# Kernel tuning notes

Measured on AMD Instinct MI355X. Metric: run time of the kernel, lower is better.

## Reference

```python
import jax, jax.numpy as jnp
import numpy as np

ALPHA = 1.0
MIN_FEATURE_SIZE = 1.0
SC = 1e-12                      # stabilizer added to first derivatives
EPS_V_FLOOR = 1e-32 / 6.0       # torch.tensor(1e-32 ** 1 / 6) == 1e-32/6 (** binds tighter than /)


def _grad2d(phi, d):
    """Vectorized equivalent of numerical_gradient_2d: central differences in the
    interior, one-sided forward/backward differences at the boundaries."""
    gx = jnp.concatenate([
        (phi[1:2, :] - phi[0:1, :]) / d,           # forward diff at i == 0
        (phi[2:, :] - phi[:-2, :]) / (2.0 * d),    # central diff in interior
        (phi[-1:, :] - phi[-2:-1, :]) / d,         # backward diff at i == H-1
    ], axis=0)
    gy = jnp.concatenate([
        (phi[:, 1:2] - phi[:, 0:1]) / d,
        (phi[:, 2:] - phi[:, :-2]) / (2.0 * d),
        (phi[:, -1:] - phi[:, -2:-1]) / d,
    ], axis=1)
    return gx, gy


def setup_inputs() -> dict:
    key = jax.random.key(0)
    eps = jax.random.normal(key, (4096, 4096), dtype=jnp.float32)
    grid_size = jnp.asarray(0.05, dtype=jnp.float32)
    return {"eps": eps, "grid_size": grid_size}


def reference(eps, grid_size):
    # mirror the field along axis 1 (torch.cat((eps, eps.flip(1)), dim=1)) -> [H, 2W]
    eps = jnp.concatenate([eps, eps[:, ::-1]], axis=1)

    # ls_derivatives: first derivatives (+SC), then second derivatives of those
    eps_x, eps_y = _grad2d(eps, grid_size)
    eps_x = eps_x + SC
    eps_y = eps_y + SC
    eps_xx, eps_xy = _grad2d(eps_x, grid_size)
    _, eps_yy = _grad2d(eps_y, grid_size)

    pi_d = np.pi / (1.1 * MIN_FEATURE_SIZE)
    eps_v = jnp.maximum(jnp.sqrt(eps_x**2 + eps_y**2), EPS_V_FLOOR)
    k = (eps_x**2 * eps_yy - 2.0 * eps_x * eps_y * eps_xy + eps_y**2 * eps_xx) / eps_v**3
    curve_const = jnp.abs(k * jnp.arctan(eps_v / eps)) - pi_d
    return jnp.nansum(ALPHA * jnp.maximum(curve_const, 0.0) * grid_size**2)
```

## Files before the change

kernel.cpp:

```cpp
#include <hip/hip_runtime.h>
#include <math.h>


#define BLOCK_X 256
#define ROWS_PER 16

__device__ __forceinline__ float fast_atan_ratio(float v, float c, float rv)
{
    const float rc = __builtin_amdgcn_rcpf(c);
    const float q  = v * rc;
    const float iq = c * rv;
    const bool  big = fabsf(q) > 1.0f;
    const float t  = big ? iq : q;
    const float s  = t * t;
    float p = fmaf(s, -0.01172120f, 0.05265332f);
    p = fmaf(s, p, -0.11643287f);
    p = fmaf(s, p,  0.19354346f);
    p = fmaf(s, p, -0.33262347f);
    p = fmaf(s, p,  0.99997726f);
    const float at = p * t;
    const float hp = copysignf(1.57079632679f, q);
    return big ? (hp - at) : at;
}

template<bool INT>
__device__ __forceinline__ float compute_rows(
    const float* __restrict__ eps, int Hn, int Wn, int i0,
    int j, int jm, int jmm, int cjp, int cjpp,
    float rd, float syj, float sym, float syp)
{
    const float rd2 = 0.5f * rd;
    const float SC = 1e-12f;
    const float FLOORV = (float)(1e-32 / 6.0);
    const float pi_d = 3.14159265358979323846f / 1.1f;

    float acc = 0.0f;
    for (int r = 0; r < ROWS_PER; ++r) {
        const int i = i0 + r;
        int im, ip, imm, ipp;
        float sxi, sxm, sxp;
        if (INT) {
            im = i - 1; ip = i + 1; imm = i - 2; ipp = i + 2;
            sxi = rd2; sxm = rd2; sxp = rd2;
        } else {
            im  = (i > 0) ? i - 1 : 0;
            ip  = (i < Hn - 1) ? i + 1 : Hn - 1;
            imm = (im > 0) ? im - 1 : 0;
            ipp = (ip < Hn - 1) ? ip + 1 : Hn - 1;
            sxi = (i == 0 || i == Hn - 1) ? rd : rd2;
            sxm = (im == 0) ? rd : rd2;
            sxp = (ip == Hn - 1) ? rd : rd2;
        }

        const float* rowc  = eps + (size_t)i   * (size_t)Wn;
        const float* rown  = eps + (size_t)im  * (size_t)Wn;
        const float* rows_ = eps + (size_t)ip  * (size_t)Wn;
        const float* rownn = eps + (size_t)imm * (size_t)Wn;
        const float* rowss = eps + (size_t)ipp * (size_t)Wn;

        const float e_c  = rowc[j];
        const float e_n  = rown[j],   e_s  = rows_[j];
        const float e_nn = rownn[j],  e_ss = rowss[j];
        const float e_w  = rowc[jm],  e_e  = rowc[cjp];
        const float e_ww = rowc[jmm], e_ee = rowc[cjpp];
        const float e_nw = rown[jm],  e_ne = rown[cjp];
        const float e_sw = rows_[jm], e_se = rows_[cjp];

        const float ex = fmaf(e_s - e_n, sxi, SC);
        const float ey = fmaf(e_e - e_w, syj, SC);

        float exn = fmaf(e_c - e_nn, sxm, SC);
        float exs = fmaf(e_ss - e_c, sxp, SC);
        if (!INT) {
            if (i == 0)      exn = ex;
            if (i == Hn - 1) exs = ex;
        }
        const float exx = (exs - exn) * sxi;

        float eyw = fmaf(e_c - e_ww, sym, SC);
        const float eye = fmaf(e_ee - e_c, syp, SC);
        if (j == 0) eyw = ey;
        const float eyy = (eye - eyw) * syj;

        const float exy = ((e_se - e_ne) - (e_sw - e_nw)) * (sxi * syj);

        const float t1 = ex * ex;
        const float t2 = ey * ey;
        float num = t1 * eyy;
        num = fmaf(t2, exx, num);
        num = fmaf(-2.0f * (ex * ey), exy, num);

        float ev = __builtin_amdgcn_sqrtf(t1 + t2);
        ev = fmaxf(ev, FLOORV);
        const float rv = __builtin_amdgcn_rcpf(ev);
        const float k  = num * (rv * rv) * rv;
        const float at = fast_atan_ratio(ev, e_c, rv);
        const float cc = fabsf(k * at) - pi_d;
        acc += fmaxf(cc, 0.0f);
    }
    return acc;
}

__global__ __launch_bounds__(BLOCK_X) void curve_partial_kernel(
    const float* __restrict__ eps, const float* __restrict__ gs,
    double* __restrict__ partial, int Hn, int Wn)
{
    const int tx = threadIdx.x;
    const int j  = blockIdx.x * BLOCK_X + tx;
    const int i0 = blockIdx.y * ROWS_PER;
    const float d  = gs[0];
    const float rd = 1.0f / d;
    const float rd2 = 0.5f * rd;

    float accf = 0.0f;
    {
        const int jm  = (j > 0) ? j - 1 : 0;
        const int jmm = (j > 1) ? j - 2 : 0;
        const int jp = j + 1, jpp = j + 2;
        const int cjp  = (jp  < Wn) ? jp  : (2 * Wn - 1 - jp);
        const int cjpp = (jpp < Wn) ? jpp : (2 * Wn - 1 - jpp);
        const float syj = (j == 0)  ? rd : rd2;
        const float sym = (jm == 0) ? rd : rd2;
        const float syp = rd2;

        const bool interior = (i0 >= 2) && (i0 + ROWS_PER + 1 < Hn);
        if (interior)
            accf = compute_rows<true >(eps, Hn, Wn, i0, j, jm, jmm, cjp, cjpp, rd, syj, sym, syp);
        else
            accf = compute_rows<false>(eps, Hn, Wn, i0, j, jm, jmm, cjp, cjpp, rd, syj, sym, syp);
    }

    double acc = (double)accf;
    #pragma unroll
    for (int off = 32; off > 0; off >>= 1)
        acc += __shfl_down(acc, off, 64);
    __shared__ double lds[BLOCK_X / 64];
    const int lane = tx & 63, wv = tx >> 6;
    if (lane == 0) lds[wv] = acc;
    __syncthreads();
    if (tx == 0) {
        partial[blockIdx.y * gridDim.x + blockIdx.x] =
            lds[0] + lds[1] + lds[2] + lds[3];
    }
}

__global__ __launch_bounds__(256) void curve_finish_kernel(
    const double* __restrict__ partial, int n,
    const float* __restrict__ gs, float* __restrict__ out)
{
    const int tx = threadIdx.x;
    double acc = 0.0;
    for (int idx = tx; idx < n; idx += 256) acc += partial[idx];
    #pragma unroll
    for (int off = 32; off > 0; off >>= 1)
        acc += __shfl_down(acc, off, 64);
    __shared__ double lds[4];
    const int lane = tx & 63, wv = tx >> 6;
    if (lane == 0) lds[wv] = acc;
    __syncthreads();
    if (tx == 0) {
        const double d = (double)gs[0];
        out[0] = (float)((lds[0] + lds[1] + lds[2] + lds[3]) * 2.0 * d * d);
    }
}

extern "C" void kernel_launch(void* const* d_in, const int* in_sizes, int n_in,
                              void* d_out, int out_size, void* d_ws, size_t ws_size,
                              hipStream_t stream) {
    const float* eps = (const float*)d_in[0];
    const float* gs  = (const float*)d_in[1];
    float* out = (float*)d_out;

    const int n = in_sizes[0];
    int Wn = (int)(sqrt((double)n) + 0.5);
    int Hn = n / Wn;

    const int gx = (Wn + BLOCK_X - 1) / BLOCK_X;
    const int gy = (Hn + ROWS_PER - 1) / ROWS_PER;
    double* partial = (double*)d_ws;

    curve_partial_kernel<<<dim3(gx, gy), BLOCK_X, 0, stream>>>(eps, gs, partial, Hn, Wn);
    curve_finish_kernel<<<1, 256, 0, stream>>>(partial, gx * gy, gs, out);
}
```

Baseline: 118.7 us.

## Register-tile 4 columns per thread with rolling 5-row window and vector loads

Each thread now computes a strip of 4 adjacent columns, keeping a rolling window of five 8-wide rows in registers that is loaded with float4/float2 vector loads. This replaces the roughly 13 scalar gathers per point with about 2 vector loads per row, cutting load instructions and address arithmetic. Rows per block drop from 16 to 8. The grid width now assumes Wn is divisible by 1024 and that accesses are 16-byte aligned, so it relies on the input shape.

```diff
diff --git a/kernel.cpp b/kernel.cpp
--- a/kernel.cpp
+++ b/kernel.cpp
@@ -3,7 +3,8 @@
 
 
 #define BLOCK_X 256
-#define ROWS_PER 16
+#define COLS 4
+#define ROWS_PER 8
 
 __device__ __forceinline__ float fast_atan_ratio(float v, float c, float rv)
 {
@@ -23,80 +24,112 @@
     return big ? (hp - at) : at;
 }
 
-template<bool INT>
-__device__ __forceinline__ float compute_rows(
-    const float* __restrict__ eps, int Hn, int Wn, int i0,
-    int j, int jm, int jmm, int cjp, int cjpp,
-    float rd, float syj, float sym, float syp)
-{
-    const float rd2 = 0.5f * rd;
-    const float SC = 1e-12f;
+__device__ __forceinline__ void load_row8(float h8[8], const float* __restrict__ rowp,
+                                          bool left, bool right)
+{
+    const float4 v = *reinterpret_cast<const float4*>(rowp);
+    float2 lo, hi;
+    if (left)  { lo.x = v.x; lo.y = v.x; }
+    else         lo = *reinterpret_cast<const float2*>(rowp - 2);
+    if (right) { hi.x = v.w; hi.y = v.z; }
+    else         hi = *reinterpret_cast<const float2*>(rowp + 4);
+    h8[0]=lo.x; h8[1]=lo.y; h8[2]=v.x; h8[3]=v.y; h8[4]=v.z; h8[5]=v.w; h8[6]=hi.x; h8[7]=hi.y;
+}
+
+__device__ __forceinline__ float point_cc(
+    const float* A, const float* B, const float* C, const float* D, const float* E,
+    int m, float sxi, float sxm, float sxp, float syj, float sym, float syp,
+    bool jz, bool itop, bool ibot)
+{
+    const float SC     = 1e-12f;
     const float FLOORV = (float)(1e-32 / 6.0);
-    const float pi_d = 3.14159265358979323846f / 1.1f;
+    const float pi_d   = 3.14159265358979323846f / 1.1f;
+
+    const float ex = fmaf(D[m] - B[m], sxi, SC);
+    const float ey = fmaf(C[m+1] - C[m-1], syj, SC);
+    float exn = fmaf(C[m] - A[m], sxm, SC);
+    float exs = fmaf(E[m] - C[m], sxp, SC);
+    if (itop) exn = ex;
+    if (ibot) exs = ex;
+    const float exx = (exs - exn) * sxi;
+    float eyw = fmaf(C[m] - C[m-2], sym, SC);
+    const float eye = fmaf(C[m+2] - C[m], syp, SC);
+    if (jz) eyw = ey;
+    const float eyy = (eye - eyw) * syj;
+    const float exy = ((D[m+1] - B[m+1]) - (D[m-1] - B[m-1])) * (sxi * syj);
+
+    const float t1 = ex * ex, t2 = ey * ey;
+    float num = t1 * eyy;
+    num = fmaf(t2, exx, num);
+    num = fmaf(-2.0f * (ex * ey), exy, num);
+    float ev = __builtin_amdgcn_sqrtf(t1 + t2);
+    ev = fmaxf(ev, FLOORV);
+    const float rv = __builtin_amdgcn_rcpf(ev);
+    const float k  = num * (rv * rv) * rv;
+    const float at = fast_atan_ratio(ev, C[m], rv);
+    const float cc = fabsf(k * at) - pi_d;
+    return fmaxf(cc, 0.0f);
+}
+
+template<bool YB>
+__device__ __forceinline__ float strip_compute(
+    const float* __restrict__ eps, int Hn, int Wn, int i0, int c,
+    bool left, bool right, float rd, float rd2)
+{
+    const float syj0 = left ? rd : rd2;
+    const float sym1 = left ? rd : rd2;
+
+    float h[5][8];
+    const float* base = eps + c;
+    const float* pr = YB ? base : (base + (ptrdiff_t)(i0 - 2) * Wn);
+
+    #pragma unroll
+    for (int q = 0; q < 4; ++q) {
+        const float* p;
+        if (YB) {
+            int t = i0 - 2 + q;
+            t = t < 0 ? 0 : t;
+            t = t > Hn - 1 ? Hn - 1 : t;
+            p = base + (size_t)t * (size_t)Wn;
+        } else {
+            p = pr;
+        }
+        load_row8(h[q], p, left, right);
+        if (!YB) pr += Wn;
+    }
 
     float acc = 0.0f;
+    #pragma unroll
     for (int r = 0; r < ROWS_PER; ++r) {
-        const int i = i0 + r;
-        int im, ip, imm, ipp;
-        float sxi, sxm, sxp;
-        if (INT) {
-            im = i - 1; ip = i + 1; imm = i - 2; ipp = i + 2;
-            sxi = rd2; sxm = rd2; sxp = rd2;
+        const float* p;
+        if (YB) {
+            int t = i0 + r + 2;
+            t = t > Hn - 1 ? Hn - 1 : t;
+            p = base + (size_t)t * (size_t)Wn;
         } else {
-            im  = (i > 0) ? i - 1 : 0;
-            ip  = (i < Hn - 1) ? i + 1 : Hn - 1;
-            imm = (im > 0) ? im - 1 : 0;
-            ipp = (ip < Hn - 1) ? ip + 1 : Hn - 1;
-            sxi = (i == 0 || i == Hn - 1) ? rd : rd2;
-            sxm = (im == 0) ? rd : rd2;
-            sxp = (ip == Hn - 1) ? rd : rd2;
+            p = pr;
         }
-
-        const float* rowc  = eps + (size_t)i   * (size_t)Wn;
-        const float* rown  = eps + (size_t)im  * (size_t)Wn;
-        const float* rows_ = eps + (size_t)ip  * (size_t)Wn;
-        const float* rownn = eps + (size_t)imm * (size_t)Wn;
-        const float* rowss = eps + (size_t)ipp * (size_t)Wn;
-
-        const float e_c  = rowc[j];
-        const float e_n  = rown[j],   e_s  = rows_[j];
-        const float e_nn = rownn[j],  e_ss = rowss[j];
-        const float e_w  = rowc[jm],  e_e  = rowc[cjp];
-        const float e_ww = rowc[jmm], e_ee = rowc[cjpp];
-        const float e_nw = rown[jm],  e_ne = rown[cjp];
-        const float e_sw = rows_[jm], e_se = rows_[cjp];
-
-        const float ex = fmaf(e_s - e_n, sxi, SC);
-        const float ey = fmaf(e_e - e_w, syj, SC);
-
-        float exn = fmaf(e_c - e_nn, sxm, SC);
-        float exs = fmaf(e_ss - e_c, sxp, SC);
-        if (!INT) {
-            if (i == 0)      exn = ex;
-            if (i == Hn - 1) exs = ex;
+        load_row8(h[(r + 4) % 5], p, left, right);
+        if (!YB) pr += Wn;
+
+        float sxi = rd2, sxm = rd2, sxp = rd2;
+        bool itop = false, ibot = false;
+        if (YB) {
+            const int i = i0 + r;
+            itop = (i == 0); ibot = (i == Hn - 1);
+            sxi = (itop || ibot) ? rd : rd2;
+            sxm = (i == 1) ? rd : rd2;
+            sxp = (i == Hn - 2) ? rd : rd2;
         }
-        const float exx = (exs - exn) * sxi;
-
-        float eyw = fmaf(e_c - e_ww, sym, SC);
-        const float eye = fmaf(e_ee - e_c, syp, SC);
-        if (j == 0) eyw = ey;
-        const float eyy = (eye - eyw) * syj;
-
-        const float exy = ((e_se - e_ne) - (e_sw - e_nw)) * (sxi * syj);
-
-        const float t1 = ex * ex;
-        const float t2 = ey * ey;
-        float num = t1 * eyy;
-        num = fmaf(t2, exx, num);
-        num = fmaf(-2.0f * (ex * ey), exy, num);
-
-        float ev = __builtin_amdgcn_sqrtf(t1 + t2);
-        ev = fmaxf(ev, FLOORV);
-        const float rv = __builtin_amdgcn_rcpf(ev);
-        const float k  = num * (rv * rv) * rv;
-        const float at = fast_atan_ratio(ev, e_c, rv);
-        const float cc = fabsf(k * at) - pi_d;
-        acc += fmaxf(cc, 0.0f);
+        const float* A = h[(r + 0) % 5];
+        const float* B = h[(r + 1) % 5];
+        const float* C = h[(r + 2) % 5];
+        const float* D = h[(r + 3) % 5];
+        const float* E = h[(r + 4) % 5];
+        acc += point_cc(A, B, C, D, E, 2, sxi, sxm, sxp, syj0, rd2,  rd2, left,  itop, ibot);
+        acc += point_cc(A, B, C, D, E, 3, sxi, sxm, sxp, rd2,  sym1, rd2, false, itop, ibot);
+        acc += point_cc(A, B, C, D, E, 4, sxi, sxm, sxp, rd2,  rd2,  rd2, false, itop, ibot);
+        acc += point_cc(A, B, C, D, E, 5, sxi, sxm, sxp, rd2,  rd2,  rd2, false, itop, ibot);
     }
     return acc;
 }
@@ -106,29 +139,18 @@
     double* __restrict__ partial, int Hn, int Wn)
 {
     const int tx = threadIdx.x;
-    const int j  = blockIdx.x * BLOCK_X + tx;
+    const int c  = (blockIdx.x * BLOCK_X + tx) * COLS;
     const int i0 = blockIdx.y * ROWS_PER;
-    const float d  = gs[0];
-    const float rd = 1.0f / d;
+    const float d   = gs[0];
+    const float rd  = 1.0f / d;
     const float rd2 = 0.5f * rd;
-
-    float accf = 0.0f;
-    {
-        const int jm  = (j > 0) ? j - 1 : 0;
-        const int jmm = (j > 1) ? j - 2 : 0;
-        const int jp = j + 1, jpp = j + 2;
-        const int cjp  = (jp  < Wn) ? jp  : (2 * Wn - 1 - jp);
-        const int cjpp = (jpp < Wn) ? jpp : (2 * Wn - 1 - jpp);
-        const float syj = (j == 0)  ? rd : rd2;
-        const float sym = (jm == 0) ? rd : rd2;
-        const float syp = rd2;
-
-        const bool interior = (i0 >= 2) && (i0 + ROWS_PER + 1 < Hn);
-        if (interior)
-            accf = compute_rows<true >(eps, Hn, Wn, i0, j, jm, jmm, cjp, cjpp, rd, syj, sym, syp);
-        else
-            accf = compute_rows<false>(eps, Hn, Wn, i0, j, jm, jmm, cjp, cjpp, rd, syj, sym, syp);
-    }
+    const bool left  = (c == 0);
+    const bool right = (c + COLS == Wn);
+
+    const bool yint = (i0 >= 2) && (i0 + ROWS_PER + 1 < Hn);
+    const float accf = yint
+        ? strip_compute<false>(eps, Hn, Wn, i0, c, left, right, rd, rd2)
+        : strip_compute<true >(eps, Hn, Wn, i0, c, left, right, rd, rd2);
 
     double acc = (double)accf;
     #pragma unroll
@@ -159,8 +181,8 @@
     if (lane == 0) lds[wv] = acc;
     __syncthreads();
     if (tx == 0) {
-        const double d = (double)gs[0];
-        out[0] = (float)((lds[0] + lds[1] + lds[2] + lds[3]) * 2.0 * d * d);
+        const double dd = (double)gs[0];
+        out[0] = (float)((lds[0] + lds[1] + lds[2] + lds[3]) * 2.0 * dd * dd);
     }
 }
 
@@ -175,7 +197,7 @@
     int Wn = (int)(sqrt((double)n) + 0.5);
     int Hn = n / Wn;
 
-    const int gx = (Wn + BLOCK_X - 1) / BLOCK_X;
+    const int gx = Wn / (BLOCK_X * COLS);
     const int gy = (Hn + ROWS_PER - 1) / ROWS_PER;
     double* partial = (double*)d_ws;
 
```

Result: slower. 128.4 us (+8.1%).

## Slide register window down rows to reuse stencil loads across iterations

Applied to the files above, without the earlier changes.

Each thread now keeps a rolling register window of the vertical and diagonal stencil values and loads only five new values per row, down from thirteen. The row loop is fully unrolled with software prefetch of the next row's values, and launch bounds now request 8 blocks per SM. The goal is fewer global/L1 load instructions and better latency hiding, at the cost of more registers and extra clamp logic in boundary blocks.

```diff
diff --git a/kernel.cpp b/kernel.cpp
--- a/kernel.cpp
+++ b/kernel.cpp
@@ -23,112 +23,119 @@
     return big ? (hp - at) : at;
 }
 
-template<bool INT>
-__device__ __forceinline__ float compute_rows(
+template<bool YB>
+__device__ __forceinline__ float strip_compute(
     const float* __restrict__ eps, int Hn, int Wn, int i0,
     int j, int jm, int jmm, int cjp, int cjpp,
-    float rd, float syj, float sym, float syp)
+    float rd, float rd2, float syj, float sym, bool jz)
 {
-    const float rd2 = 0.5f * rd;
-    const float SC = 1e-12f;
+    const float SC     = 1e-12f;
     const float FLOORV = (float)(1e-32 / 6.0);
-    const float pi_d = 3.14159265358979323846f / 1.1f;
+    const float pi_d   = 3.14159265358979323846f / 1.1f;
+
+    auto rp = [&](int t) -> const float* {
+        int tt = t;
+        if (YB) { tt = tt < 0 ? 0 : tt; tt = tt > Hn - 1 ? Hn - 1 : tt; }
+        return eps + (size_t)tt * (size_t)Wn;
+    };
+
+    float a2 = rp(i0 - 2)[j],   a1 = rp(i0 - 1)[j],  a0 = rp(i0)[j];
+    float b1 = rp(i0 + 1)[j],   b2 = rp(i0 + 2)[j];
+    float wN = rp(i0 - 1)[jm],  w0 = rp(i0)[jm],     wS = rp(i0 + 1)[jm];
+    float eN = rp(i0 - 1)[cjp], e0 = rp(i0)[cjp],    eS = rp(i0 + 1)[cjp];
+    float ww = rp(i0)[jmm],     ee = rp(i0)[cjpp];
+
+    const float* pj = eps + (size_t)(i0 + 3) * (size_t)Wn;
+    const float* p2 = eps + (size_t)(i0 + 2) * (size_t)Wn;
+    const float* p1 = eps + (size_t)(i0 + 1) * (size_t)Wn;
 
     float acc = 0.0f;
+    #pragma unroll
     for (int r = 0; r < ROWS_PER; ++r) {
         const int i = i0 + r;
-        int im, ip, imm, ipp;
-        float sxi, sxm, sxp;
-        if (INT) {
-            im = i - 1; ip = i + 1; imm = i - 2; ipp = i + 2;
-            sxi = rd2; sxm = rd2; sxp = rd2;
-        } else {
-            im  = (i > 0) ? i - 1 : 0;
-            ip  = (i < Hn - 1) ? i + 1 : Hn - 1;
-            imm = (im > 0) ? im - 1 : 0;
-            ipp = (ip < Hn - 1) ? ip + 1 : Hn - 1;
-            sxi = (i == 0 || i == Hn - 1) ? rd : rd2;
-            sxm = (im == 0) ? rd : rd2;
-            sxp = (ip == Hn - 1) ? rd : rd2;
+
+        float nb2 = 0.0f, nwS = 0.0f, neS = 0.0f, nww = 0.0f, nee = 0.0f;
+        if (r + 1 < ROWS_PER) {
+            if (YB) {
+                const float* q3 = rp(i + 3);
+                const float* q2 = rp(i + 2);
+                const float* q1 = rp(i + 1);
+                nb2 = q3[j]; nwS = q2[jm]; neS = q2[cjp];
+                nww = q1[jmm]; nee = q1[cjpp];
+            } else {
+                nb2 = pj[j]; nwS = p2[jm]; neS = p2[cjp];
+                nww = p1[jmm]; nee = p1[cjpp];
+                pj += Wn; p2 += Wn; p1 += Wn;
+            }
         }
 
-        const float* rowc  = eps + (size_t)i   * (size_t)Wn;
-        const float* rown  = eps + (size_t)im  * (size_t)Wn;
-        const float* rows_ = eps + (size_t)ip  * (size_t)Wn;
-        const float* rownn = eps + (size_t)imm * (size_t)Wn;
-        const float* rowss = eps + (size_t)ipp * (size_t)Wn;
+        float sxi = rd2, sxm = rd2, sxp = rd2;
+        bool itop = false, ibot = false;
+        if (YB) {
+            itop = (i == 0); ibot = (i == Hn - 1);
+            sxi = (itop || ibot) ? rd : rd2;
+            sxm = (i == 1) ? rd : rd2;
+            sxp = (i == Hn - 2) ? rd : rd2;
+        }
 
-        const float e_c  = rowc[j];
-        const float e_n  = rown[j],   e_s  = rows_[j];
-        const float e_nn = rownn[j],  e_ss = rowss[j];
-        const float e_w  = rowc[jm],  e_e  = rowc[cjp];
-        const float e_ww = rowc[jmm], e_ee = rowc[cjpp];
-        const float e_nw = rown[jm],  e_ne = rown[cjp];
-        const float e_sw = rows_[jm], e_se = rows_[cjp];
+        const float ex = fmaf(b1 - a1, sxi, SC);
+        const float ey = fmaf(e0 - w0, syj, SC);
+        float exn = fmaf(a0 - a2, sxm, SC);
+        float exs = fmaf(b2 - a0, sxp, SC);
+        if (YB) { if (itop) exn = ex; if (ibot) exs = ex; }
+        const float exx = (exs - exn) * sxi;
+        float eyw = fmaf(a0 - ww, sym, SC);
+        const float eye = fmaf(ee - a0, rd2, SC);
+        if (jz) eyw = ey;
+        const float eyy = (eye - eyw) * syj;
+        const float exy = ((eS - eN) - (wS - wN)) * (sxi * syj);
 
-        const float ex = fmaf(e_s - e_n, sxi, SC);
-        const float ey = fmaf(e_e - e_w, syj, SC);
-
-        float exn = fmaf(e_c - e_nn, sxm, SC);
-        float exs = fmaf(e_ss - e_c, sxp, SC);
-        if (!INT) {
-            if (i == 0)      exn = ex;
-            if (i == Hn - 1) exs = ex;
-        }
-        const float exx = (exs - exn) * sxi;
-
-        float eyw = fmaf(e_c - e_ww, sym, SC);
-        const float eye = fmaf(e_ee - e_c, syp, SC);
-        if (j == 0) eyw = ey;
-        const float eyy = (eye - eyw) * syj;
-
-        const float exy = ((e_se - e_ne) - (e_sw - e_nw)) * (sxi * syj);
-
-        const float t1 = ex * ex;
-        const float t2 = ey * ey;
+        const float t1 = ex * ex, t2 = ey * ey;
         float num = t1 * eyy;
         num = fmaf(t2, exx, num);
         num = fmaf(-2.0f * (ex * ey), exy, num);
-
         float ev = __builtin_amdgcn_sqrtf(t1 + t2);
         ev = fmaxf(ev, FLOORV);
         const float rv = __builtin_amdgcn_rcpf(ev);
         const float k  = num * (rv * rv) * rv;
-        const float at = fast_atan_ratio(ev, e_c, rv);
+        const float at = fast_atan_ratio(ev, a0, rv);
         const float cc = fabsf(k * at) - pi_d;
-        acc += fmaxf(cc, 0.0f);
+        float contrib = fmaxf(cc, 0.0f);
+        if (YB && i >= Hn) contrib = 0.0f;
+        acc += contrib;
+
+        a2 = a1; a1 = a0; a0 = b1; b1 = b2; b2 = nb2;
+        wN = w0; w0 = wS; wS = nwS;
+        eN = e0; e0 = eS; eS = neS;
+        ww = nww; ee = nee;
     }
     return acc;
 }
 
-__global__ __launch_bounds__(BLOCK_X) void curve_partial_kernel(
+__global__ __launch_bounds__(BLOCK_X, 8) void curve_partial_kernel(
     const float* __restrict__ eps, const float* __restrict__ gs,
     double* __restrict__ partial, int Hn, int Wn)
 {
     const int tx = threadIdx.x;
     const int j  = blockIdx.x * BLOCK_X + tx;
     const int i0 = blockIdx.y * ROWS_PER;
-    const float d  = gs[0];
-    const float rd = 1.0f / d;
+    const float d   = gs[0];
+    const float rd  = 1.0f / d;
     const float rd2 = 0.5f * rd;
 
-    float accf = 0.0f;
-    {
-        const int jm  = (j > 0) ? j - 1 : 0;
-        const int jmm = (j > 1) ? j - 2 : 0;
-        const int jp = j + 1, jpp = j + 2;
-        const int cjp  = (jp  < Wn) ? jp  : (2 * Wn - 1 - jp);
-        const int cjpp = (jpp < Wn) ? jpp : (2 * Wn - 1 - jpp);
-        const float syj = (j == 0)  ? rd : rd2;
-        const float sym = (jm == 0) ? rd : rd2;
-        const float syp = rd2;
+    const int jm  = (j > 0) ? j - 1 : 0;
+    const int jmm = (j > 1) ? j - 2 : 0;
+    const int jp = j + 1, jpp = j + 2;
+    const int cjp  = (jp  < Wn) ? jp  : (2 * Wn - 1 - jp);
+    const int cjpp = (jpp < Wn) ? jpp : (2 * Wn - 1 - jpp);
+    const bool jz = (j == 0);
+    const float syj = jz ? rd : rd2;
+    const float sym = (jm == 0) ? rd : rd2;
 
-        const bool interior = (i0 >= 2) && (i0 + ROWS_PER + 1 < Hn);
-        if (interior)
-            accf = compute_rows<true >(eps, Hn, Wn, i0, j, jm, jmm, cjp, cjpp, rd, syj, sym, syp);
-        else
-            accf = compute_rows<false>(eps, Hn, Wn, i0, j, jm, jmm, cjp, cjpp, rd, syj, sym, syp);
-    }
+    const bool yint = (i0 >= 2) && (i0 + ROWS_PER + 1 < Hn);
+    const float accf = yint
+        ? strip_compute<false>(eps, Hn, Wn, i0, j, jm, jmm, cjp, cjpp, rd, rd2, syj, sym, jz)
+        : strip_compute<true >(eps, Hn, Wn, i0, j, jm, jmm, cjp, cjpp, rd, rd2, syj, sym, jz);
 
     double acc = (double)accf;
     #pragma unroll
@@ -159,8 +166,8 @@
     if (lane == 0) lds[wv] = acc;
     __syncthreads();
     if (tx == 0) {
-        const double d = (double)gs[0];
-        out[0] = (float)((lds[0] + lds[1] + lds[2] + lds[3]) * 2.0 * d * d);
+        const double dd = (double)gs[0];
+        out[0] = (float)((lds[0] + lds[1] + lds[2] + lds[3]) * 2.0 * dd * dd);
     }
 }
 
```

Measured after the change: 155.3 us. +30.8%, slower.
